# Performance work log

Hardware: AMD Instinct MI355X
Metric: run time of the kernel (lower is better)

Reference implementation:

```python
import jax, jax.numpy as jnp
import numpy as np

N = 100000
E = 1600000
F_IN = 128
HID = 64
N_CLS = 16


def gcn_conv(x, row, col, W, b, n_nodes):
    # x: [N, Fin]; row/col: [E+N] (self-loops already appended)
    h = x @ W  # [N, Fout]
    ones = jnp.ones(row.shape[0], dtype=x.dtype)
    deg = jax.ops.segment_sum(ones, col, num_segments=n_nodes)  # in-degree incl. self-loop
    dinv = jnp.where(deg > 0, jax.lax.rsqrt(deg), 0.0)
    norm = dinv[row] * dinv[col]  # [E+N]
    msg = h[row] * norm[:, None]  # gather + scale
    out = jax.ops.segment_sum(msg, col, num_segments=n_nodes)  # scatter-add
    return out + b


def setup_inputs() -> dict:
    key = jax.random.key(0)
    k1, k2, k3, k4, k5, k6 = jax.random.split(key, 6)
    x = jax.random.normal(k1, (N, F_IN), dtype=jnp.float32)
    edge_index = jax.random.randint(k2, (2, E), 0, N, dtype=jnp.int64)
    # Glorot-ish init for weights
    W1 = jax.random.normal(k3, (F_IN, HID), dtype=jnp.float32) / np.sqrt(F_IN)
    b1 = jnp.zeros((HID,), dtype=jnp.float32)
    W2 = jax.random.normal(k4, (HID, N_CLS), dtype=jnp.float32) / np.sqrt(HID)
    b2 = jnp.zeros((N_CLS,), dtype=jnp.float32)
    return {"x": x, "edge_index": edge_index, "W1": W1, "b1": b1, "W2": W2, "b2": b2}


def reference(x, edge_index, W1, b1, W2, b2):
    # Add self-loops (GCNConv default add_self_loops=True)
    loop = jnp.arange(N, dtype=edge_index.dtype)
    row = jnp.concatenate([edge_index[0], loop])
    col = jnp.concatenate([edge_index[1], loop])
    h = gcn_conv(x, row, col, W1, b1, N)
    h = jax.nn.relu(h)
    h = gcn_conv(h, row, col, W2, b2, N)
    return jax.nn.log_softmax(h, axis=1)
```

## Files before the change

### kernel.cpp

```cpp
#include <hip/hip_runtime.h>
#include <hip/hip_fp16.h>

#define F_IN 128
#define HID  64
#define NCLS 16
#define NPB  128
#define CAP  4096
#define CHUNK 4096
#define BINTHREADS 1024

typedef _Float16 half_t;
typedef __attribute__((ext_vector_type(8))) _Float16 half8;
typedef __attribute__((ext_vector_type(4))) float float4v;


__global__ __launch_bounds__(BINTHREADS) void phaseA(
    const int* __restrict__ row, const int* __restrict__ col,
    int* __restrict__ cursor, int* __restrict__ ebuf, int E, int NB,
    const float* __restrict__ W1, half_t* __restrict__ W1t, int nblkE)
{
    if ((int)blockIdx.x >= nblkE) {
        for (int i = threadIdx.x; i < F_IN * HID; i += BINTHREADS) {
            int k = i >> 6, n = i & 63;
            W1t[n * F_IN + k] = (half_t)W1[i];
        }
        return;
    }
    __shared__ int hist[1024], base[1024], off[1024];
    for (int i = threadIdx.x; i < NB; i += BINTHREADS) hist[i] = 0;
    int e0 = blockIdx.x * CHUNK + threadIdx.x * 4;
    int nv = min(max(E - e0, 0), 4);
    int4 c4 = make_int4(0, 0, 0, 0), r4 = make_int4(0, 0, 0, 0);
    if (nv == 4) {
        c4 = *(const int4*)&col[e0];
        r4 = *(const int4*)&row[e0];
    } else {
        if (nv > 0) { c4.x = col[e0 + 0]; r4.x = row[e0 + 0]; }
        if (nv > 1) { c4.y = col[e0 + 1]; r4.y = row[e0 + 1]; }
        if (nv > 2) { c4.z = col[e0 + 2]; r4.z = row[e0 + 2]; }
    }
    __syncthreads();
    if (nv > 0) atomicAdd(&hist[c4.x >> 7], 1);
    if (nv > 1) atomicAdd(&hist[c4.y >> 7], 1);
    if (nv > 2) atomicAdd(&hist[c4.z >> 7], 1);
    if (nv > 3) atomicAdd(&hist[c4.w >> 7], 1);
    __syncthreads();
    for (int i = threadIdx.x; i < NB; i += BINTHREADS) {
        int h = hist[i];
        base[i] = h ? (i * CAP + atomicAdd(&cursor[i], h)) : 0;
        off[i] = 0;
    }
    __syncthreads();
    if (nv > 0) { int b = c4.x >> 7; int p = base[b] + atomicAdd(&off[b], 1);
                  if (p < (b + 1) * CAP) ebuf[p] = (r4.x << 7) | (c4.x & (NPB - 1)); }
    if (nv > 1) { int b = c4.y >> 7; int p = base[b] + atomicAdd(&off[b], 1);
                  if (p < (b + 1) * CAP) ebuf[p] = (r4.y << 7) | (c4.y & (NPB - 1)); }
    if (nv > 2) { int b = c4.z >> 7; int p = base[b] + atomicAdd(&off[b], 1);
                  if (p < (b + 1) * CAP) ebuf[p] = (r4.z << 7) | (c4.z & (NPB - 1)); }
    if (nv > 3) { int b = c4.w >> 7; int p = base[b] + atomicAdd(&off[b], 1);
                  if (p < (b + 1) * CAP) ebuf[p] = (r4.w << 7) | (c4.w & (NPB - 1)); }
}


__global__ __launch_bounds__(256) void csr_gemm1(
    const int* __restrict__ ebuf, const int* __restrict__ cursor,
    const float* __restrict__ x, const half_t* __restrict__ W1t,
    int2* __restrict__ rsc, int* __restrict__ csr_row,
    __half* __restrict__ hs1, int N, int NG)
{
    __shared__ int hist[NPB];
    __shared__ float dv[NPB];
    int t = threadIdx.x;

    if ((int)blockIdx.x < NG) {
        int b = blockIdx.x;
        int node0 = b << 7;
        int ebase = b * CAP;
        int p[8];
        #pragma unroll
        for (int k = 0; k < 8; ++k) p[k] = ebuf[ebase + t + 256 * k];
        int cnt = min(cursor[b], CAP);
        if (t < NPB) hist[t] = 0;
        __syncthreads();
        #pragma unroll
        for (int k = 0; k < 8; ++k)
            if (t + 256 * k < cnt) atomicAdd(&hist[p[k] & (NPB - 1)], 1);
        if (cnt > 2048)
            for (int e = 2048 + t; e < cnt; e += 256)
                atomicAdd(&hist[ebuf[ebase + e] & (NPB - 1)], 1);
        __syncthreads();
        if (t < NPB) dv[t] = rsqrtf((float)hist[t] + 1.0f);
        __syncthreads();

        int wv = t >> 6, lane = t & 63;
        int l15 = lane & 15, quad = lane >> 4;
        int mbase = wv * 32;
        int r0 = min(node0 + mbase + l15, N - 1);
        int r1 = min(node0 + mbase + 16 + l15, N - 1);
        const float* x0 = x + (size_t)r0 * F_IN;
        const float* x1 = x + (size_t)r1 * F_IN;
        float4v acc[2][4];
        #pragma unroll
        for (int mt = 0; mt < 2; ++mt)
            #pragma unroll
            for (int j = 0; j < 4; ++j) acc[mt][j] = (float4v){0.f, 0.f, 0.f, 0.f};
        #pragma unroll
        for (int kb = 0; kb < 4; ++kb) {
            int off = kb * 32 + quad * 8;
            float4 fa = *(const float4*)&x0[off];
            float4 fb = *(const float4*)&x0[off + 4];
            float4 ga = *(const float4*)&x1[off];
            float4 gb = *(const float4*)&x1[off + 4];
            half8 a0 = {(half_t)fa.x, (half_t)fa.y, (half_t)fa.z, (half_t)fa.w,
                        (half_t)fb.x, (half_t)fb.y, (half_t)fb.z, (half_t)fb.w};
            half8 a1 = {(half_t)ga.x, (half_t)ga.y, (half_t)ga.z, (half_t)ga.w,
                        (half_t)gb.x, (half_t)gb.y, (half_t)gb.z, (half_t)gb.w};
            #pragma unroll
            for (int j = 0; j < 4; ++j) {
                half8 bv = *(const half8*)&W1t[(size_t)(j * 16 + l15) * F_IN + off];
                acc[0][j] = __builtin_amdgcn_mfma_f32_16x16x32_f16(a0, bv, acc[0][j], 0, 0, 0);
                acc[1][j] = __builtin_amdgcn_mfma_f32_16x16x32_f16(a1, bv, acc[1][j], 0, 0, 0);
            }
        }
        #pragma unroll
        for (int mt = 0; mt < 2; ++mt)
            #pragma unroll
            for (int j = 0; j < 4; ++j)
                #pragma unroll
                for (int r = 0; r < 4; ++r) {
                    int m = mbase + mt * 16 + quad * 4 + r;
                    int n = node0 + m;
                    if (n < N) hs1[(size_t)n * HID + j * 16 + l15] =
                        __float2half(acc[mt][j][r] * dv[m]);
                }
        return;
    }

    __shared__ int cur[NPB];
    __shared__ int wtot;
    int b = blockIdx.x - NG;
    int node0 = b << 7;
    int ebase = b * CAP;
    int p[8];
    #pragma unroll
    for (int k = 0; k < 8; ++k) p[k] = ebuf[ebase + t + 256 * k];
    int cnt = min(cursor[b], CAP);
    if (t < NPB) hist[t] = 0;
    __syncthreads();
    #pragma unroll
    for (int k = 0; k < 8; ++k)
        if (t + 256 * k < cnt) atomicAdd(&hist[p[k] & (NPB - 1)], 1);
    if (cnt > 2048)
        for (int e = 2048 + t; e < cnt; e += 256)
            atomicAdd(&hist[ebuf[ebase + e] & (NPB - 1)], 1);
    __syncthreads();
    int h = 0, incl = 0;
    if (t < NPB) {
        h = hist[t];
        incl = h;
        #pragma unroll
        for (int off = 1; off < 64; off <<= 1) {
            int u = __shfl_up(incl, off, 64);
            if ((t & 63) >= off) incl += u;
        }
        if (t == 63) wtot = incl;
    }
    __syncthreads();
    if (t < NPB) {
        if (t >= 64) incl += wtot;
        int start = ebase + incl - h;
        cur[t] = start;
        int n = node0 + t;
        if (n < N) rsc[n] = make_int2(start, h);
    }
    __syncthreads();
    #pragma unroll
    for (int k = 0; k < 8; ++k)
        if (t + 256 * k < cnt) {
            int pos = atomicAdd(&cur[p[k] & (NPB - 1)], 1);
            csr_row[pos] = p[k] >> 7;
        }
    if (cnt > 2048)
        for (int e = 2048 + t; e < cnt; e += 256) {
            int pp = ebuf[ebase + e];
            int pos = atomicAdd(&cur[pp & (NPB - 1)], 1);
            csr_row[pos] = pp >> 7;
        }
}


__global__ __launch_bounds__(256) void agg_l1(
    const __half* __restrict__ hs1, const int2* __restrict__ rsc,
    const int* __restrict__ csr, const float* __restrict__ b1,
    const float* __restrict__ W2, __half* __restrict__ h2s, int N)
{
    __shared__ float W2l[HID * NCLS];
    __shared__ float o1[32][65];
    for (int i = threadIdx.x; i < HID * NCLS; i += 256) W2l[i] = W2[i];
    __syncthreads();
    int w = threadIdx.x >> 6, lane = threadIdx.x & 63;
    int g = lane >> 3, gl = lane & 7;
    int rowi = w * 8 + g;
    int c = blockIdx.x * 32 + rowi;
    bool active = (c < N);
    int cc = active ? c : 0;
    int2 rc = rsc[cc];
    int e0 = rc.x, e1 = rc.x + rc.y;
    int e1m1 = e1 - 1;
    float dc = rsqrtf((float)rc.y + 1.0f);
    const half8* H = (const half8*)hs1;
    half8 sv = H[(size_t)cc * 8 + gl];
    float sum[8];
    #pragma unroll
    for (int k = 0; k < 8; ++k) sum[k] = (float)sv[k];
    for (int i = e0; i < e1; i += 8) {
        int id[8];
        #pragma unroll
        for (int s = 0; s < 8; ++s) id[s] = csr[min(i + s, e1m1)];
        half8 a[8];
        #pragma unroll
        for (int s = 0; s < 8; ++s) a[s] = H[(size_t)id[s] * 8 + gl];
        #pragma unroll
        for (int s = 0; s < 8; ++s) {
            float fm = (i + s < e1) ? 1.f : 0.f;
            #pragma unroll
            for (int k = 0; k < 8; ++k) sum[k] = fmaf(fm, (float)a[s][k], sum[k]);
        }
    }
    float4 bb0 = *(const float4*)&b1[gl * 8];
    float4 bb1 = *(const float4*)&b1[gl * 8 + 4];
    o1[rowi][gl * 8 + 0] = fmaxf(fmaf(dc, sum[0], bb0.x), 0.f);
    o1[rowi][gl * 8 + 1] = fmaxf(fmaf(dc, sum[1], bb0.y), 0.f);
    o1[rowi][gl * 8 + 2] = fmaxf(fmaf(dc, sum[2], bb0.z), 0.f);
    o1[rowi][gl * 8 + 3] = fmaxf(fmaf(dc, sum[3], bb0.w), 0.f);
    o1[rowi][gl * 8 + 4] = fmaxf(fmaf(dc, sum[4], bb1.x), 0.f);
    o1[rowi][gl * 8 + 5] = fmaxf(fmaf(dc, sum[5], bb1.y), 0.f);
    o1[rowi][gl * 8 + 6] = fmaxf(fmaf(dc, sum[6], bb1.z), 0.f);
    o1[rowi][gl * 8 + 7] = fmaxf(fmaf(dc, sum[7], bb1.w), 0.f);
    int j0 = gl * 2, j1 = gl * 2 + 1;
    float s0 = 0.f, s1 = 0.f;
    const float* orow = o1[rowi];
    #pragma unroll 8
    for (int k = 0; k < HID; ++k) {
        float ov = orow[k];
        s0 = fmaf(ov, W2l[k * NCLS + j0], s0);
        s1 = fmaf(ov, W2l[k * NCLS + j1], s1);
    }
    if (active) {
        __half2 hv;
        hv.x = __float2half(dc * s0);
        hv.y = __float2half(dc * s1);
        ((__half2*)h2s)[(size_t)c * 8 + gl] = hv;
    }
}


__global__ __launch_bounds__(256) void agg2_final(
    const __half* __restrict__ h2s, const int2* __restrict__ rsc,
    const int* __restrict__ csr, const float* __restrict__ b2,
    float* __restrict__ out, int N)
{
    int lane = threadIdx.x & 63;
    int g = lane >> 3, gl = lane & 7;
    int c = blockIdx.x * 32 + (threadIdx.x >> 6) * 8 + g;
    bool active = (c < N);
    int cc = active ? c : 0;
    int2 rc = rsc[cc];
    int e0 = rc.x, e1 = rc.x + rc.y;
    int e1m1 = e1 - 1;
    float dcv = rsqrtf((float)rc.y + 1.0f);
    const __half2* H = (const __half2*)h2s;
    float2 sum = __half22float2(H[(size_t)cc * 8 + gl]);
    for (int i = e0; i < e1; i += 8) {
        int id[8];
        #pragma unroll
        for (int s = 0; s < 8; ++s) id[s] = csr[min(i + s, e1m1)];
        __half2 a[8];
        #pragma unroll
        for (int s = 0; s < 8; ++s) a[s] = H[(size_t)id[s] * 8 + gl];
        #pragma unroll
        for (int s = 0; s < 8; ++s) {
            float fm = (i + s < e1) ? 1.f : 0.f;
            float2 f2 = __half22float2(a[s]);
            sum.x = fmaf(fm, f2.x, sum.x);
            sum.y = fmaf(fm, f2.y, sum.y);
        }
    }
    float2 bb = ((const float2*)b2)[gl];
    float2 v;
    v.x = fmaf(dcv, sum.x, bb.x);
    v.y = fmaf(dcv, sum.y, bb.y);
    float mx = fmaxf(v.x, v.y);
    mx = fmaxf(mx, __shfl_xor(mx, 1, 64));
    mx = fmaxf(mx, __shfl_xor(mx, 2, 64));
    mx = fmaxf(mx, __shfl_xor(mx, 4, 64));
    float s = __expf(v.x - mx) + __expf(v.y - mx);
    s += __shfl_xor(s, 1, 64);
    s += __shfl_xor(s, 2, 64);
    s += __shfl_xor(s, 4, 64);
    float lse = mx + __logf(s);
    if (active) ((float2*)out)[(size_t)c * 8 + gl] = make_float2(v.x - lse, v.y - lse);
}


extern "C" void kernel_launch(void* const* d_in, const int* in_sizes, int n_in,
                              void* d_out, int out_size, void* d_ws, size_t ws_size,
                              hipStream_t stream) {
    const float* x  = (const float*)d_in[0];
    const int*   ei = (const int*)d_in[1];
    const float* W1 = (const float*)d_in[2];
    const float* b1 = (const float*)d_in[3];
    const float* W2 = (const float*)d_in[4];
    const float* b2 = (const float*)d_in[5];
    float* out = (float*)d_out;

    const int N = in_sizes[0] / F_IN;
    const int E = in_sizes[1] / 2;
    const int* row = ei;
    const int* col = ei + E;

    const int NB = (N + NPB - 1) / NPB;
    size_t Np  = ((size_t)N + 15) & ~(size_t)15;
    size_t NBp = ((size_t)NB + 15) & ~(size_t)15;
    size_t Rg  = (size_t)NB * CAP;

    char* p = (char*)d_ws;
    __half* hs1     = (__half*)p;  p += Np * HID * 2;
    __half* h2s     = (__half*)p;  p += Np * NCLS * 2;
    half_t* W1t     = (half_t*)p;  p += (size_t)F_IN * HID * 2;
    int2*   rsc     = (int2*)p;    p += Np * 8;
    int*    csr_row = (int*)p;     p += Rg * 4;
    int*    ebuf    = (int*)p;     p += Rg * 4;
    int*    cursor  = (int*)p;     p += NBp * 4;

    int nblkE = (E + CHUNK - 1) / CHUNK;

    hipMemsetAsync(cursor, 0, NBp * sizeof(int), stream);
    phaseA<<<nblkE + 1, BINTHREADS, 0, stream>>>(row, col, cursor, ebuf, E, NB, W1, W1t, nblkE);
    csr_gemm1<<<2 * NB, 256, 0, stream>>>(ebuf, cursor, x, W1t, rsc, csr_row, hs1, N, NB);
    agg_l1<<<(N + 31) / 32, 256, 0, stream>>>(hs1, rsc, csr_row, b1, W2, h2s, N);
    agg2_final<<<(N + 31) / 32, 256, 0, stream>>>(h2s, rsc, csr_row, b2, out, N);
}
```

Measured before the change: 184.1 us.

## Merge CSR build and GEMM blocks; add fp16 tree-sum full-chunk aggregation loops

The csr_gemm1 kernel used separate block groups for the degree/GEMM path and the CSR-building path, and each group loaded ebuf and built the histogram on its own. Now each block builds the histogram once, writes the CSR rows, derives dinv from the same histogram, and then runs the MFMA GEMM, so the grid is half as large and the duplicate histogram work is gone. The two aggregation kernels also gain an unmasked loop for full 8-edge chunks that sums the gathered features in fp16 with a pairwise tree before adding to the fp32 accumulator, and a masked tail handles the remainder. The fp16 partial sums lose some precision, and the merged blocks carry longer serial work with less parallelism.

```diff
diff --git a/kernel.cpp b/kernel.cpp
--- a/kernel.cpp
+++ b/kernel.cpp
@@ -66,81 +66,17 @@
     const int* __restrict__ ebuf, const int* __restrict__ cursor,
     const float* __restrict__ x, const half_t* __restrict__ W1t,
     int2* __restrict__ rsc, int* __restrict__ csr_row,
-    __half* __restrict__ hs1, int N, int NG)
+    __half* __restrict__ hs1, int N)
 {
     __shared__ int hist[NPB];
     __shared__ float dv[NPB];
-    int t = threadIdx.x;
-
-    if ((int)blockIdx.x < NG) {
-        int b = blockIdx.x;
-        int node0 = b << 7;
-        int ebase = b * CAP;
-        int p[8];
-        #pragma unroll
-        for (int k = 0; k < 8; ++k) p[k] = ebuf[ebase + t + 256 * k];
-        int cnt = min(cursor[b], CAP);
-        if (t < NPB) hist[t] = 0;
-        __syncthreads();
-        #pragma unroll
-        for (int k = 0; k < 8; ++k)
-            if (t + 256 * k < cnt) atomicAdd(&hist[p[k] & (NPB - 1)], 1);
-        if (cnt > 2048)
-            for (int e = 2048 + t; e < cnt; e += 256)
-                atomicAdd(&hist[ebuf[ebase + e] & (NPB - 1)], 1);
-        __syncthreads();
-        if (t < NPB) dv[t] = rsqrtf((float)hist[t] + 1.0f);
-        __syncthreads();
-
-        int wv = t >> 6, lane = t & 63;
-        int l15 = lane & 15, quad = lane >> 4;
-        int mbase = wv * 32;
-        int r0 = min(node0 + mbase + l15, N - 1);
-        int r1 = min(node0 + mbase + 16 + l15, N - 1);
-        const float* x0 = x + (size_t)r0 * F_IN;
-        const float* x1 = x + (size_t)r1 * F_IN;
-        float4v acc[2][4];
-        #pragma unroll
-        for (int mt = 0; mt < 2; ++mt)
-            #pragma unroll
-            for (int j = 0; j < 4; ++j) acc[mt][j] = (float4v){0.f, 0.f, 0.f, 0.f};
-        #pragma unroll
-        for (int kb = 0; kb < 4; ++kb) {
-            int off = kb * 32 + quad * 8;
-            float4 fa = *(const float4*)&x0[off];
-            float4 fb = *(const float4*)&x0[off + 4];
-            float4 ga = *(const float4*)&x1[off];
-            float4 gb = *(const float4*)&x1[off + 4];
-            half8 a0 = {(half_t)fa.x, (half_t)fa.y, (half_t)fa.z, (half_t)fa.w,
-                        (half_t)fb.x, (half_t)fb.y, (half_t)fb.z, (half_t)fb.w};
-            half8 a1 = {(half_t)ga.x, (half_t)ga.y, (half_t)ga.z, (half_t)ga.w,
-                        (half_t)gb.x, (half_t)gb.y, (half_t)gb.z, (half_t)gb.w};
-            #pragma unroll
-            for (int j = 0; j < 4; ++j) {
-                half8 bv = *(const half8*)&W1t[(size_t)(j * 16 + l15) * F_IN + off];
-                acc[0][j] = __builtin_amdgcn_mfma_f32_16x16x32_f16(a0, bv, acc[0][j], 0, 0, 0);
-                acc[1][j] = __builtin_amdgcn_mfma_f32_16x16x32_f16(a1, bv, acc[1][j], 0, 0, 0);
-            }
-        }
-        #pragma unroll
-        for (int mt = 0; mt < 2; ++mt)
-            #pragma unroll
-            for (int j = 0; j < 4; ++j)
-                #pragma unroll
-                for (int r = 0; r < 4; ++r) {
-                    int m = mbase + mt * 16 + quad * 4 + r;
-                    int n = node0 + m;
-                    if (n < N) hs1[(size_t)n * HID + j * 16 + l15] =
-                        __float2half(acc[mt][j][r] * dv[m]);
-                }
-        return;
-    }
-
     __shared__ int cur[NPB];
     __shared__ int wtot;
-    int b = blockIdx.x - NG;
+    int t = threadIdx.x;
+    int b = blockIdx.x;
     int node0 = b << 7;
     int ebase = b * CAP;
+
     int p[8];
     #pragma unroll
     for (int k = 0; k < 8; ++k) p[k] = ebuf[ebase + t + 256 * k];
@@ -154,6 +90,7 @@
         for (int e = 2048 + t; e < cnt; e += 256)
             atomicAdd(&hist[ebuf[ebase + e] & (NPB - 1)], 1);
     __syncthreads();
+
     int h = 0, incl = 0;
     if (t < NPB) {
         h = hist[t];
@@ -172,8 +109,10 @@
         cur[t] = start;
         int n = node0 + t;
         if (n < N) rsc[n] = make_int2(start, h);
-    }
-    __syncthreads();
+        dv[t] = rsqrtf((float)h + 1.0f);
+    }
+    __syncthreads();
+
     #pragma unroll
     for (int k = 0; k < 8; ++k)
         if (t + 256 * k < cnt) {
@@ -186,6 +125,48 @@
             int pos = atomicAdd(&cur[pp & (NPB - 1)], 1);
             csr_row[pos] = pp >> 7;
         }
+
+    int wv = t >> 6, lane = t & 63;
+    int l15 = lane & 15, quad = lane >> 4;
+    int mbase = wv * 32;
+    int r0 = min(node0 + mbase + l15, N - 1);
+    int r1 = min(node0 + mbase + 16 + l15, N - 1);
+    const float* x0 = x + (size_t)r0 * F_IN;
+    const float* x1 = x + (size_t)r1 * F_IN;
+    float4v acc[2][4];
+    #pragma unroll
+    for (int mt = 0; mt < 2; ++mt)
+        #pragma unroll
+        for (int j = 0; j < 4; ++j) acc[mt][j] = (float4v){0.f, 0.f, 0.f, 0.f};
+    #pragma unroll
+    for (int kb = 0; kb < 4; ++kb) {
+        int off = kb * 32 + quad * 8;
+        float4 fa = *(const float4*)&x0[off];
+        float4 fb = *(const float4*)&x0[off + 4];
+        float4 ga = *(const float4*)&x1[off];
+        float4 gb = *(const float4*)&x1[off + 4];
+        half8 a0 = {(half_t)fa.x, (half_t)fa.y, (half_t)fa.z, (half_t)fa.w,
+                    (half_t)fb.x, (half_t)fb.y, (half_t)fb.z, (half_t)fb.w};
+        half8 a1 = {(half_t)ga.x, (half_t)ga.y, (half_t)ga.z, (half_t)ga.w,
+                    (half_t)gb.x, (half_t)gb.y, (half_t)gb.z, (half_t)gb.w};
+        #pragma unroll
+        for (int j = 0; j < 4; ++j) {
+            half8 bv = *(const half8*)&W1t[(size_t)(j * 16 + l15) * F_IN + off];
+            acc[0][j] = __builtin_amdgcn_mfma_f32_16x16x32_f16(a0, bv, acc[0][j], 0, 0, 0);
+            acc[1][j] = __builtin_amdgcn_mfma_f32_16x16x32_f16(a1, bv, acc[1][j], 0, 0, 0);
+        }
+    }
+    #pragma unroll
+    for (int mt = 0; mt < 2; ++mt)
+        #pragma unroll
+        for (int j = 0; j < 4; ++j)
+            #pragma unroll
+            for (int r = 0; r < 4; ++r) {
+                int m = mbase + mt * 16 + quad * 4 + r;
+                int n = node0 + m;
+                if (n < N) hs1[(size_t)n * HID + j * 16 + l15] =
+                    __float2half(acc[mt][j][r] * dv[m]);
+            }
 }
 
 
@@ -206,14 +187,32 @@
     int cc = active ? c : 0;
     int2 rc = rsc[cc];
     int e0 = rc.x, e1 = rc.x + rc.y;
-    int e1m1 = e1 - 1;
     float dc = rsqrtf((float)rc.y + 1.0f);
     const half8* H = (const half8*)hs1;
     half8 sv = H[(size_t)cc * 8 + gl];
     float sum[8];
     #pragma unroll
     for (int k = 0; k < 8; ++k) sum[k] = (float)sv[k];
-    for (int i = e0; i < e1; i += 8) {
+    int i = e0;
+    for (; i + 8 <= e1; i += 8) {
+        int id[8];
+        #pragma unroll
+        for (int s = 0; s < 8; ++s) id[s] = csr[i + s];
+        half8 a[8];
+        #pragma unroll
+        for (int s = 0; s < 8; ++s) a[s] = H[(size_t)id[s] * 8 + gl];
+        half8 t0 = a[0] + a[1];
+        half8 t1 = a[2] + a[3];
+        half8 t2 = a[4] + a[5];
+        half8 t3 = a[6] + a[7];
+        half8 u0 = t0 + t1;
+        half8 u1 = t2 + t3;
+        half8 v = u0 + u1;
+        #pragma unroll
+        for (int k = 0; k < 8; ++k) sum[k] += (float)v[k];
+    }
+    if (i < e1) {
+        int e1m1 = e1 - 1;
         int id[8];
         #pragma unroll
         for (int s = 0; s < 8; ++s) id[s] = csr[min(i + s, e1m1)];
@@ -267,11 +266,28 @@
     int cc = active ? c : 0;
     int2 rc = rsc[cc];
     int e0 = rc.x, e1 = rc.x + rc.y;
-    int e1m1 = e1 - 1;
     float dcv = rsqrtf((float)rc.y + 1.0f);
     const __half2* H = (const __half2*)h2s;
     float2 sum = __half22float2(H[(size_t)cc * 8 + gl]);
-    for (int i = e0; i < e1; i += 8) {
+    int i = e0;
+    for (; i + 8 <= e1; i += 8) {
+        int id[8];
+        #pragma unroll
+        for (int s = 0; s < 8; ++s) id[s] = csr[i + s];
+        __half2 a[8];
+        #pragma unroll
+        for (int s = 0; s < 8; ++s) a[s] = H[(size_t)id[s] * 8 + gl];
+        __half2 t0 = __hadd2(a[0], a[1]);
+        __half2 t1 = __hadd2(a[2], a[3]);
+        __half2 t2 = __hadd2(a[4], a[5]);
+        __half2 t3 = __hadd2(a[6], a[7]);
+        __half2 v = __hadd2(__hadd2(t0, t1), __hadd2(t2, t3));
+        float2 f2 = __half22float2(v);
+        sum.x += f2.x;
+        sum.y += f2.y;
+    }
+    if (i < e1) {
+        int e1m1 = e1 - 1;
         int id[8];
         #pragma unroll
         for (int s = 0; s < 8; ++s) id[s] = csr[min(i + s, e1m1)];
@@ -337,7 +353,7 @@
 
     hipMemsetAsync(cursor, 0, NBp * sizeof(int), stream);
     phaseA<<<nblkE + 1, BINTHREADS, 0, stream>>>(row, col, cursor, ebuf, E, NB, W1, W1t, nblkE);
-    csr_gemm1<<<2 * NB, 256, 0, stream>>>(ebuf, cursor, x, W1t, rsc, csr_row, hs1, N, NB);
+    csr_gemm1<<<NB, 256, 0, stream>>>(ebuf, cursor, x, W1t, rsc, csr_row, hs1, N);
     agg_l1<<<(N + 31) / 32, 256, 0, stream>>>(hs1, rsc, csr_row, b1, W2, h2s, N);
     agg2_final<<<(N + 31) / 32, 256, 0, stream>>>(h2s, rsc, csr_row, b2, out, N);
 }
```

New measurement: 192.1 us. +4.3%, slower.

## Split full/tail edge loops, sum in fp16 tree, remap layer-2 aggregation lanes

Applied to the files above, without the earlier changes.

Both aggregation kernels now run a clean unmasked loop over full groups of 8 edges and handle the remainder separately. Each group of 8 gathered rows is reduced with a packed half-precision add tree before being accumulated in fp32, which cuts conversion and FMA work. The layer-2 kernel now gives each node 2 lanes that each load half8 instead of 8 lanes loading half2, so a block covers 128 nodes with wider gathers and fewer shuffles. The half-precision partial sums lose some accuracy compared with accumulating every edge in fp32.

```diff
diff --git a/kernel.cpp b/kernel.cpp
--- a/kernel.cpp
+++ b/kernel.cpp
@@ -206,14 +206,32 @@
     int cc = active ? c : 0;
     int2 rc = rsc[cc];
     int e0 = rc.x, e1 = rc.x + rc.y;
-    int e1m1 = e1 - 1;
     float dc = rsqrtf((float)rc.y + 1.0f);
     const half8* H = (const half8*)hs1;
     half8 sv = H[(size_t)cc * 8 + gl];
     float sum[8];
     #pragma unroll
     for (int k = 0; k < 8; ++k) sum[k] = (float)sv[k];
-    for (int i = e0; i < e1; i += 8) {
+    int i = e0;
+    for (; i + 8 <= e1; i += 8) {
+        int id[8];
+        #pragma unroll
+        for (int s = 0; s < 8; ++s) id[s] = csr[i + s];
+        half8 a[8];
+        #pragma unroll
+        for (int s = 0; s < 8; ++s) a[s] = H[(size_t)id[s] * 8 + gl];
+        half8 t0 = a[0] + a[1];
+        half8 t1 = a[2] + a[3];
+        half8 t2 = a[4] + a[5];
+        half8 t3 = a[6] + a[7];
+        half8 u0 = t0 + t1;
+        half8 u1 = t2 + t3;
+        half8 v = u0 + u1;
+        #pragma unroll
+        for (int k = 0; k < 8; ++k) sum[k] += (float)v[k];
+    }
+    if (i < e1) {
+        int e1m1 = e1 - 1;
         int id[8];
         #pragma unroll
         for (int s = 0; s < 8; ++s) id[s] = csr[min(i + s, e1m1)];
@@ -260,46 +278,73 @@
     const int* __restrict__ csr, const float* __restrict__ b2,
     float* __restrict__ out, int N)
 {
-    int lane = threadIdx.x & 63;
-    int g = lane >> 3, gl = lane & 7;
-    int c = blockIdx.x * 32 + (threadIdx.x >> 6) * 8 + g;
+    int t = threadIdx.x;
+    int w = t >> 6, lane = t & 63;
+    int nw = lane >> 1, hl = lane & 1;
+    int c = blockIdx.x * 128 + w * 32 + nw;
     bool active = (c < N);
     int cc = active ? c : 0;
     int2 rc = rsc[cc];
     int e0 = rc.x, e1 = rc.x + rc.y;
-    int e1m1 = e1 - 1;
     float dcv = rsqrtf((float)rc.y + 1.0f);
-    const __half2* H = (const __half2*)h2s;
-    float2 sum = __half22float2(H[(size_t)cc * 8 + gl]);
-    for (int i = e0; i < e1; i += 8) {
+    const half8* H = (const half8*)h2s;
+    half8 sv = H[(size_t)cc * 2 + hl];
+    float sum[8];
+    #pragma unroll
+    for (int k = 0; k < 8; ++k) sum[k] = (float)sv[k];
+    int i = e0;
+    for (; i + 8 <= e1; i += 8) {
         int id[8];
         #pragma unroll
+        for (int s = 0; s < 8; ++s) id[s] = csr[i + s];
+        half8 a[8];
+        #pragma unroll
+        for (int s = 0; s < 8; ++s) a[s] = H[(size_t)id[s] * 2 + hl];
+        half8 t0 = a[0] + a[1];
+        half8 t1 = a[2] + a[3];
+        half8 t2 = a[4] + a[5];
+        half8 t3 = a[6] + a[7];
+        half8 v = (t0 + t1) + (t2 + t3);
+        #pragma unroll
+        for (int k = 0; k < 8; ++k) sum[k] += (float)v[k];
+    }
+    if (i < e1) {
+        int e1m1 = e1 - 1;
+        int id[8];
+        #pragma unroll
         for (int s = 0; s < 8; ++s) id[s] = csr[min(i + s, e1m1)];
-        __half2 a[8];
-        #pragma unroll
-        for (int s = 0; s < 8; ++s) a[s] = H[(size_t)id[s] * 8 + gl];
+        half8 a[8];
+        #pragma unroll
+        for (int s = 0; s < 8; ++s) a[s] = H[(size_t)id[s] * 2 + hl];
         #pragma unroll
         for (int s = 0; s < 8; ++s) {
             float fm = (i + s < e1) ? 1.f : 0.f;
-            float2 f2 = __half22float2(a[s]);
-            sum.x = fmaf(fm, f2.x, sum.x);
-            sum.y = fmaf(fm, f2.y, sum.y);
-        }
-    }
-    float2 bb = ((const float2*)b2)[gl];
-    float2 v;
-    v.x = fmaf(dcv, sum.x, bb.x);
-    v.y = fmaf(dcv, sum.y, bb.y);
-    float mx = fmaxf(v.x, v.y);
+            #pragma unroll
+            for (int k = 0; k < 8; ++k) sum[k] = fmaf(fm, (float)a[s][k], sum[k]);
+        }
+    }
+    float4 bb0 = *(const float4*)&b2[hl * 8];
+    float4 bb1 = *(const float4*)&b2[hl * 8 + 4];
+    float v0 = fmaf(dcv, sum[0], bb0.x);
+    float v1 = fmaf(dcv, sum[1], bb0.y);
+    float v2 = fmaf(dcv, sum[2], bb0.z);
+    float v3 = fmaf(dcv, sum[3], bb0.w);
+    float v4 = fmaf(dcv, sum[4], bb1.x);
+    float v5 = fmaf(dcv, sum[5], bb1.y);
+    float v6 = fmaf(dcv, sum[6], bb1.z);
+    float v7 = fmaf(dcv, sum[7], bb1.w);
+    float mx = fmaxf(fmaxf(fmaxf(v0, v1), fmaxf(v2, v3)),
+                     fmaxf(fmaxf(v4, v5), fmaxf(v6, v7)));
     mx = fmaxf(mx, __shfl_xor(mx, 1, 64));
-    mx = fmaxf(mx, __shfl_xor(mx, 2, 64));
-    mx = fmaxf(mx, __shfl_xor(mx, 4, 64));
-    float s = __expf(v.x - mx) + __expf(v.y - mx);
+    float s = __expf(v0 - mx) + __expf(v1 - mx) + __expf(v2 - mx) + __expf(v3 - mx)
+            + __expf(v4 - mx) + __expf(v5 - mx) + __expf(v6 - mx) + __expf(v7 - mx);
     s += __shfl_xor(s, 1, 64);
-    s += __shfl_xor(s, 2, 64);
-    s += __shfl_xor(s, 4, 64);
     float lse = mx + __logf(s);
-    if (active) ((float2*)out)[(size_t)c * 8 + gl] = make_float2(v.x - lse, v.y - lse);
+    if (active) {
+        float* o = out + (size_t)c * NCLS + hl * 8;
+        *(float4*)&o[0] = make_float4(v0 - lse, v1 - lse, v2 - lse, v3 - lse);
+        *(float4*)&o[4] = make_float4(v4 - lse, v5 - lse, v6 - lse, v7 - lse);
+    }
 }
 
 
@@ -339,5 +384,5 @@
     phaseA<<<nblkE + 1, BINTHREADS, 0, stream>>>(row, col, cursor, ebuf, E, NB, W1, W1t, nblkE);
     csr_gemm1<<<2 * NB, 256, 0, stream>>>(ebuf, cursor, x, W1t, rsc, csr_row, hs1, N, NB);
     agg_l1<<<(N + 31) / 32, 256, 0, stream>>>(hs1, rsc, csr_row, b1, W2, h2s, N);
-    agg2_final<<<(N + 31) / 32, 256, 0, stream>>>(h2s, rsc, csr_row, b2, out, N);
-}
+    agg2_final<<<(N + 127) / 128, 256, 0, stream>>>(h2s, rsc, csr_row, b2, out, N);
+}
```

New measurement: 182.0 us. About the same (-1.2%).
